# Optimization experiments

Measured on AMD Instinct MI355X. Metric: run time of the kernel, lower is better.

## Reference

```python
import jax, jax.numpy as jnp
import numpy as np

# Segment geometry (from init_kwargs): modes ['u','uv','v'] -> out_v = alpha * x_u @ W_uv
U = 128
V = 128
IN_OFF = [0, 128, 256, 384]
W_OFF = [k * U * V for k in range(8)]          # [0,16384,...,114688]
OUT_OFF = [0, 128, 256, 384]
IN_STRIDE = 512
OUT_STRIDE = 512
W_STRIDE = 8 * U * V                           # 131072
# (in_seg, w_seg, out_seg, coefficient)
PATHS = [(0, 0, 0, 1.0), (1, 1, 1, 1.0), (2, 2, 2, 1.0), (3, 3, 3, 1.0),
         (0, 4, 1, 0.5), (1, 5, 2, 0.5), (2, 6, 3, 0.5), (3, 7, 0, 0.5)]
B = 32768
E = 4  # num_embeddings (experts)


def setup_inputs() -> dict:
    key = jax.random.key(0)
    k1, k2, k3 = jax.random.split(key, 3)
    tensor_in = jax.random.normal(k1, (B, IN_STRIDE), dtype=jnp.float32)
    tensor_w = jax.random.normal(k2, (E, W_STRIDE), dtype=jnp.float32)
    tensor_w_id = jax.random.randint(k3, (B,), 0, E, dtype=jnp.int32)
    return {"tensor_in": tensor_in, "tensor_w": tensor_w, "tensor_w_id": tensor_w_id}


def _batch_linear(tensor_in, tensor_w, tensor_w_id):
    """Segmented path-indexed grouped linear (cuEquivariance BatchLinear fwd).

    tensor_in: [B, IN_STRIDE]; tensor_w: [E, W_STRIDE]; tensor_w_id: [B] int in [0,E).
    For each path (i, j, k, alpha):
        out[b, OUT_OFF[k]:+V] += alpha * x[b, IN_OFF[i]:+U] @ W[w_id[b], seg j].reshape(U, V)
    """
    nb = tensor_in.shape[0]
    ne = tensor_w.shape[0]
    onehot = jax.nn.one_hot(tensor_w_id, ne, dtype=tensor_in.dtype)  # [B, E]
    out = jnp.zeros((nb, OUT_STRIDE), dtype=tensor_in.dtype)
    for (i, j, k, a) in PATHS:
        x = tensor_in[:, IN_OFF[i]:IN_OFF[i] + U]                    # [B, U]
        w_seg = tensor_w[:, W_OFF[j]:W_OFF[j] + U * V].reshape(ne, U, V)
        # masked per-expert dense GEMMs (small fixed expert count)
        y = jnp.zeros((nb, V), dtype=tensor_in.dtype)
        for e in range(ne):
            y = y + onehot[:, e:e + 1] * (x @ w_seg[e])              # [B, V]
        out = out.at[:, OUT_OFF[k]:OUT_OFF[k] + V].add(a * y)
    return out


def reference(tensor_in, tensor_w, tensor_w_id):
    return _batch_linear(tensor_in, tensor_w, tensor_w_id)
```

## Files before the change

### kernel.cpp

```cpp
#include <hip/hip_runtime.h>
#include <stdint.h>

#define U 128
#define V 128
#define IN_STRIDE 512
#define OUT_STRIDE 512
#define W_STRIDE (8 * U * V)
#define NB 32768
#define MAXTILES 1027

#define WS_WSHUF 0
#define WS_PERM  (1 << 20)
#define WS_CURS  ((1 << 20) + (1 << 19))
#define WS_XSHUF (2 << 20)

typedef __bf16 bf16x8 __attribute__((ext_vector_type(8)));
typedef float f32x16 __attribute__((ext_vector_type(16)));
typedef unsigned int u32x4 __attribute__((ext_vector_type(4)));

static __device__ __forceinline__ unsigned short f2bf(float f) {
    unsigned int u = __builtin_bit_cast(unsigned int, f);
    u += 0x7FFFu + ((u >> 16) & 1u);
    return (unsigned short)(u >> 16);
}

static __device__ __forceinline__ void tile_map(int g, int c0, int c1, int c2, int c3,
                                                int& e, int& rows, int& tbase) {
    int cs[4] = {c0, c1, c2, c3};
    int acc = 0; e = -1; rows = 0; tbase = 0;
#pragma unroll
    for (int i = 0; i < 4; i++) {
        int te = (cs[i] + 31) >> 5;
        if (e < 0 && g < acc + te) {
            e = i;
            int tile = g - acc;
            rows = cs[i] - tile * 32;
            if (rows > 32) rows = 32;
            tbase = i * NB + tile * 32;
        }
        acc += te;
    }
}

__global__ void prep_kernel(const float* __restrict__ w, const int* __restrict__ wid,
                            unsigned short* __restrict__ wshuf, int* __restrict__ cursors,
                            int* __restrict__ perm) {
    int blk = blockIdx.x;
    if (blk < 256) {
        int t = blk * 256 + threadIdx.x;
        int lane = t & 63;
        int kt = (t >> 6) & 7;
        int nt = (t >> 9) & 3;
        int s  = (t >> 11) & 7;
        int e  = (t >> 14) & 3;
        int kbase = kt * 16 + ((lane >> 5) << 3);
        int n = nt * 32 + (lane & 31);
        const float* src = w + (size_t)e * W_STRIDE + (size_t)s * (U * V) + n;
        float sc = (s >= 4) ? 0.5f : 1.0f;
        __attribute__((aligned(16))) unsigned short o[8];
#pragma unroll
        for (int j = 0; j < 8; j++) o[j] = f2bf(src[(size_t)(kbase + j) * V] * sc);
        *(u32x4*)(wshuf + (size_t)t * 8) = *(const u32x4*)o;
    } else {
        __shared__ int lcnt[4], lbase[4];
        int tid = threadIdx.x;
        if (tid < 4) lcnt[tid] = 0;
        __syncthreads();
        int b = (blk - 256) * 256 + tid;
        int e = wid[b];
        int r = atomicAdd(&lcnt[e], 1);
        __syncthreads();
        if (tid < 4) lbase[tid] = atomicAdd(&cursors[tid], lcnt[tid]);
        __syncthreads();
        perm[e * NB + lbase[e] + r] = b;
    }
}

__global__ __launch_bounds__(256, 4) void xshuf_kernel(
        const float* __restrict__ x, const int* __restrict__ perm,
        const int* __restrict__ cursors, unsigned short* __restrict__ xshuf) {
    int t = blockIdx.x * 256 + threadIdx.x;
    int tile = t >> 11;
    int rem = t & 2047;
    int ktile = rem >> 6;
    int lane = rem & 63;
    int c0 = cursors[0], c1 = cursors[1], c2 = cursors[2], c3 = cursors[3];
    int e, rows, tbase;
    tile_map(tile, c0, c1, c2, c3, e, rows, tbase);
    int m = lane & 31;
    __attribute__((aligned(16))) unsigned short o[8] = {0, 0, 0, 0, 0, 0, 0, 0};
    if (e >= 0 && m < rows) {
        int row = perm[tbase + m];
        const float* p = x + (size_t)row * IN_STRIDE + ktile * 16 + ((lane >> 5) << 3);
        float4 v0 = *(const float4*)p;
        float4 v1 = *(const float4*)(p + 4);
        o[0] = f2bf(v0.x); o[1] = f2bf(v0.y); o[2] = f2bf(v0.z); o[3] = f2bf(v0.w);
        o[4] = f2bf(v1.x); o[5] = f2bf(v1.y); o[6] = f2bf(v1.z); o[7] = f2bf(v1.w);
    }
    *(u32x4*)(xshuf + (size_t)t * 8) = *(const u32x4*)o;
}

__global__ __launch_bounds__(256, 4) void gemm_kernel(
        const unsigned short* __restrict__ xshuf, const unsigned short* __restrict__ wshuf,
        const int* __restrict__ cursors, const int* __restrict__ perm,
        float* __restrict__ out) {
    int c0 = cursors[0], c1 = cursors[1], c2 = cursors[2], c3 = cursors[3];
    int g = blockIdx.x;
    int e, rows, tbase;
    tile_map(g, c0, c1, c2, c3, e, rows, tbase);
    if (e < 0) return;

    const int t = threadIdx.x;
    const int kout = t >> 6;
    const int lane = t & 63;
    const int m0 = lane & 31;

    const unsigned short* xs = xshuf + (size_t)g * 16384;

    f32x16 acc0 = {}, acc1 = {}, acc2 = {}, acc3 = {};

    const int xb0 = kout, sg0 = kout;
    const int xb1 = (kout + 3) & 3, sg1 = xb1 + 4;
    int xbs[2] = {xb0, xb1};
    int sgs[2] = {sg0, sg1};

#pragma unroll
    for (int c = 0; c < 2; c++) {
        const unsigned short* wbase = wshuf + (size_t)(e * 8 + sgs[c]) * 16384;
        const int Kbase = xbs[c] * 8;
#pragma unroll
        for (int kt = 0; kt < 8; kt++) {
            bf16x8 a = __builtin_bit_cast(bf16x8,
                *(const u32x4*)(xs + ((size_t)(Kbase + kt) * 64 + lane) * 8));
            bf16x8 b0 = __builtin_bit_cast(bf16x8,
                *(const u32x4*)(wbase + ((size_t)(0 * 8 + kt) * 64 + lane) * 8));
            bf16x8 b1 = __builtin_bit_cast(bf16x8,
                *(const u32x4*)(wbase + ((size_t)(1 * 8 + kt) * 64 + lane) * 8));
            bf16x8 b2 = __builtin_bit_cast(bf16x8,
                *(const u32x4*)(wbase + ((size_t)(2 * 8 + kt) * 64 + lane) * 8));
            bf16x8 b3 = __builtin_bit_cast(bf16x8,
                *(const u32x4*)(wbase + ((size_t)(3 * 8 + kt) * 64 + lane) * 8));
            acc0 = __builtin_amdgcn_mfma_f32_32x32x16_bf16(a, b0, acc0, 0, 0, 0);
            acc1 = __builtin_amdgcn_mfma_f32_32x32x16_bf16(a, b1, acc1, 0, 0, 0);
            acc2 = __builtin_amdgcn_mfma_f32_32x32x16_bf16(a, b2, acc2, 0, 0, 0);
            acc3 = __builtin_amdgcn_mfma_f32_32x32x16_bf16(a, b3, acc3, 0, 0, 0);
        }
    }

    const int rh = (lane >> 5) << 2;
    const int colb = kout * 128 + m0;
#pragma unroll
    for (int q = 0; q < 4; q++) {
#pragma unroll
        for (int d = 0; d < 4; d++) {
            int rl = d + 8 * q + rh;
            if (rl < rows) {
                int rg = perm[tbase + rl];
                float* o = out + (size_t)rg * OUT_STRIDE + colb;
                int reg = q * 4 + d;
                o[0]  = acc0[reg];
                o[32] = acc1[reg];
                o[64] = acc2[reg];
                o[96] = acc3[reg];
            }
        }
    }
}

extern "C" void kernel_launch(void* const* d_in, const int* in_sizes, int n_in,
                              void* d_out, int out_size, void* d_ws, size_t ws_size,
                              hipStream_t stream) {
    const float* x = (const float*)d_in[0];
    const float* w = (const float*)d_in[1];
    const int* wid = (const int*)d_in[2];
    float* out = (float*)d_out;

    char* ws = (char*)d_ws;
    unsigned short* wshuf = (unsigned short*)(ws + WS_WSHUF);
    int* perm = (int*)(ws + WS_PERM);
    int* cursors = (int*)(ws + WS_CURS);
    unsigned short* xshuf = (unsigned short*)(ws + WS_XSHUF);

    hipMemsetAsync(cursors, 0, 16, stream);
    prep_kernel<<<384, 256, 0, stream>>>(w, wid, wshuf, cursors, perm);
    xshuf_kernel<<<MAXTILES * 8, 256, 0, stream>>>(x, perm, cursors, xshuf);
    gemm_kernel<<<MAXTILES, 256, 0, stream>>>(xshuf, wshuf, cursors, perm, out);
}
```

Baseline: 154.9 us.

## Fuse x gather and bf16 conversion into GEMM kernel, drop xshuf pass

Removes the separate xshuf kernel, which gathered permuted rows of x, converted them to bf16 and wrote a shuffled buffer. The GEMM kernel now reads fp32 x rows directly through perm and converts to bf16 in registers before each MFMA. This saves one kernel launch plus a full write and reread of the intermediate buffer. In exchange each of the four waves rereads its own x segment in fp32 with strided per-row loads, and the launch bound drops to 3 blocks per SM.

```diff
diff --git a/kernel.cpp b/kernel.cpp
--- a/kernel.cpp
+++ b/kernel.cpp
@@ -12,7 +12,6 @@
 #define WS_WSHUF 0
 #define WS_PERM  (1 << 20)
 #define WS_CURS  ((1 << 20) + (1 << 19))
-#define WS_XSHUF (2 << 20)
 
 typedef __bf16 bf16x8 __attribute__((ext_vector_type(8)));
 typedef float f32x16 __attribute__((ext_vector_type(16)));
@@ -76,32 +75,8 @@
     }
 }
 
-__global__ __launch_bounds__(256, 4) void xshuf_kernel(
-        const float* __restrict__ x, const int* __restrict__ perm,
-        const int* __restrict__ cursors, unsigned short* __restrict__ xshuf) {
-    int t = blockIdx.x * 256 + threadIdx.x;
-    int tile = t >> 11;
-    int rem = t & 2047;
-    int ktile = rem >> 6;
-    int lane = rem & 63;
-    int c0 = cursors[0], c1 = cursors[1], c2 = cursors[2], c3 = cursors[3];
-    int e, rows, tbase;
-    tile_map(tile, c0, c1, c2, c3, e, rows, tbase);
-    int m = lane & 31;
-    __attribute__((aligned(16))) unsigned short o[8] = {0, 0, 0, 0, 0, 0, 0, 0};
-    if (e >= 0 && m < rows) {
-        int row = perm[tbase + m];
-        const float* p = x + (size_t)row * IN_STRIDE + ktile * 16 + ((lane >> 5) << 3);
-        float4 v0 = *(const float4*)p;
-        float4 v1 = *(const float4*)(p + 4);
-        o[0] = f2bf(v0.x); o[1] = f2bf(v0.y); o[2] = f2bf(v0.z); o[3] = f2bf(v0.w);
-        o[4] = f2bf(v1.x); o[5] = f2bf(v1.y); o[6] = f2bf(v1.z); o[7] = f2bf(v1.w);
-    }
-    *(u32x4*)(xshuf + (size_t)t * 8) = *(const u32x4*)o;
-}
-
-__global__ __launch_bounds__(256, 4) void gemm_kernel(
-        const unsigned short* __restrict__ xshuf, const unsigned short* __restrict__ wshuf,
+__global__ __launch_bounds__(256, 3) void gemm_kernel(
+        const float* __restrict__ x, const unsigned short* __restrict__ wshuf,
         const int* __restrict__ cursors, const int* __restrict__ perm,
         float* __restrict__ out) {
     int c0 = cursors[0], c1 = cursors[1], c2 = cursors[2], c3 = cursors[3];
@@ -114,8 +89,11 @@
     const int kout = t >> 6;
     const int lane = t & 63;
     const int m0 = lane & 31;
+    const int hi8 = (lane >> 5) << 3;
 
-    const unsigned short* xs = xshuf + (size_t)g * 16384;
+    const bool val = (m0 < rows);
+    const int row_g = val ? perm[tbase + m0] : 0;
+    const float* xrow = x + (size_t)row_g * IN_STRIDE;
 
     f32x16 acc0 = {}, acc1 = {}, acc2 = {}, acc3 = {};
 
@@ -127,11 +105,15 @@
 #pragma unroll
     for (int c = 0; c < 2; c++) {
         const unsigned short* wbase = wshuf + (size_t)(e * 8 + sgs[c]) * 16384;
-        const int Kbase = xbs[c] * 8;
+        const float* xa = xrow + xbs[c] * 128 + hi8;
 #pragma unroll
         for (int kt = 0; kt < 8; kt++) {
-            bf16x8 a = __builtin_bit_cast(bf16x8,
-                *(const u32x4*)(xs + ((size_t)(Kbase + kt) * 64 + lane) * 8));
+            float4 v0 = *(const float4*)(xa + kt * 16);
+            float4 v1 = *(const float4*)(xa + kt * 16 + 4);
+            __attribute__((aligned(16))) unsigned short ah[8];
+            ah[0] = f2bf(v0.x); ah[1] = f2bf(v0.y); ah[2] = f2bf(v0.z); ah[3] = f2bf(v0.w);
+            ah[4] = f2bf(v1.x); ah[5] = f2bf(v1.y); ah[6] = f2bf(v1.z); ah[7] = f2bf(v1.w);
+            bf16x8 a = __builtin_bit_cast(bf16x8, *(const u32x4*)ah);
             bf16x8 b0 = __builtin_bit_cast(bf16x8,
                 *(const u32x4*)(wbase + ((size_t)(0 * 8 + kt) * 64 + lane) * 8));
             bf16x8 b1 = __builtin_bit_cast(bf16x8,
@@ -179,10 +161,8 @@
     unsigned short* wshuf = (unsigned short*)(ws + WS_WSHUF);
     int* perm = (int*)(ws + WS_PERM);
     int* cursors = (int*)(ws + WS_CURS);
-    unsigned short* xshuf = (unsigned short*)(ws + WS_XSHUF);
 
     hipMemsetAsync(cursors, 0, 16, stream);
     prep_kernel<<<384, 256, 0, stream>>>(w, wid, wshuf, cursors, perm);
-    xshuf_kernel<<<MAXTILES * 8, 256, 0, stream>>>(x, perm, cursors, xshuf);
-    gemm_kernel<<<MAXTILES, 256, 0, stream>>>(xshuf, wshuf, cursors, perm, out);
+    gemm_kernel<<<MAXTILES, 256, 0, stream>>>(x, wshuf, cursors, perm, out);
 }
```

Result: no change. 154.5 us (-0.3%).
